# Optimization experiments

Hardware: AMD Instinct MI355X
Metric: run time of the kernel (lower is better)

Reference implementation:

```python
import jax, jax.numpy as jnp
import numpy as np

H, W = 640, 640
C_IN, C_OUT = 3, 64
K, PAD = 7, 3          # 7x7 sparse conv, SAME padding (stride 1)
POOL_K, POOL_S = 3, 2  # valid 3x3 max pool, stride 2
N_SITES = 100000
BN_EPS = 1e-5


def setup_inputs() -> dict:
    key = jax.random.key(0)
    k1, k2, k3 = jax.random.split(key, 3)
    feature_map = jax.random.normal(k1, (H, W, C_IN), dtype=jnp.float32)
    update_location = jax.random.randint(k2, (N_SITES, 2), 0, min(H, W)).astype(jnp.int64)
    # kaiming-uniform-ish init for the 7x7x3 -> 64 conv weight
    fan_in = K * K * C_IN
    bound = np.sqrt(3.0 / fan_in).astype(np.float32)
    weight = jax.random.uniform(k3, (K, K, C_IN, C_OUT), jnp.float32, -bound, bound)
    return {
        "update_location": update_location,
        "feature_map": feature_map,
        "weight": weight,
        "gamma": jnp.ones((C_OUT,), jnp.float32),
        "beta": jnp.zeros((C_OUT,), jnp.float32),
        "running_mean": jnp.zeros((C_OUT,), jnp.float32),
        "running_var": jnp.ones((C_OUT,), jnp.float32),
    }


def reference(update_location, feature_map, weight, gamma, beta, running_mean, running_var):
    # ---- sparse (active-site) 7x7 conv: gather patches only at active sites ----
    fm = jnp.pad(feature_map, ((PAD, PAD), (PAD, PAD), (0, 0)))  # zero pad borders
    offs = jnp.arange(K)
    rows = update_location[:, 0, None] + offs          # [N, K] (pad offset = +PAD-PAD)
    cols = update_location[:, 1, None] + offs          # [N, K]
    patches = fm[rows[:, :, None], cols[:, None, :]]   # [N, K, K, C_IN]
    feats = jnp.einsum('nijc,ijco->no', patches, weight)  # [N, C_OUT]

    # ---- frozen BN + ReLU fused on active sites ----
    inv = gamma * jax.lax.rsqrt(running_var + BN_EPS)
    feats = jnp.maximum(feats * inv + (beta - running_mean * inv), 0.0)

    # ---- scatter active-site features into dense map (inactive sites stay 0) ----
    dense = jnp.zeros((H, W, C_OUT), feats.dtype).at[
        update_location[:, 0], update_location[:, 1]].set(feats)

    # ---- 3x3 stride-2 valid max pool (ReLU outputs >= 0, zeros elsewhere) ----
    pooled = jax.lax.reduce_window(
        dense, 0.0, jax.lax.max,
        (POOL_K, POOL_K, 1), (POOL_S, POOL_S, 1), 'VALID')  # [319, 319, C_OUT]
    return pooled
```

## Files before the change

kernel.cpp:

```cpp
#include <hip/hip_runtime.h>

#define HH 640
#define WW 640
#define COUT 64
#define KK 7
#define NS 100000
#define OHh 319
#define OWw 319
#define PWY 646
#define PWX 648
#define WGT_BLKS 7
#define OWNER_BLKS 391
#define PAD_BLKS 818
#define NBLK 1563
#define NWB (4 * KK * 64)
#define TPR 40

typedef _Float16 half2_t __attribute__((ext_vector_type(2)));
typedef _Float16 h8 __attribute__((ext_vector_type(8)));
typedef float f4 __attribute__((ext_vector_type(4)));
typedef uint4 u4a __attribute__((aligned(8)));

union H2U { unsigned u; half2_t h; };
union H8U { uint4 u; h8 h; _Float16 e[8]; };

__device__ __forceinline__ unsigned short f2bf(float x) {
    unsigned u = __float_as_uint(x);
    return (unsigned short)((u + 0x7FFFu + ((u >> 16) & 1u)) >> 16);
}
__device__ __forceinline__ float bf2f(unsigned short b) {
    return __uint_as_float((unsigned)b << 16);
}

__device__ __forceinline__ bool detect_is64(const int* __restrict__ loc) {
    const int smp = loc[1 + 2 * (int)(threadIdx.x & 63)];
    return __ballot(smp != 0) == 0ULL;
}

__global__ __launch_bounds__(256) void prep_kernel(
        const int* __restrict__ loc, const float* __restrict__ fm,
        const float* __restrict__ wgt, const float* __restrict__ gamma,
        const float* __restrict__ beta, const float* __restrict__ mean,
        const float* __restrict__ var,
        int* __restrict__ owner, uint2* __restrict__ pfm,
        uint4* __restrict__ wbg, float* __restrict__ bn,
        int* __restrict__ aidx) {
    if (blockIdx.x < WGT_BLKS) {
        const int e = blockIdx.x * 256 + threadIdx.x;
        const int t = e / (KK * 64);
        const int rem = e - t * KK * 64;
        const int i = rem >> 6, l = rem & 63;
        const int cout = t * 16 + (l & 15);
        const int q = l >> 4;
        H8U w;
        #pragma unroll
        for (int j = 0; j < 8; ++j) {
            const int kl = q * 8 + j, px = kl >> 2, ci = kl & 3;
            const float v = (px < KK && ci < 3)
                              ? wgt[((i * KK + px) * 3 + ci) * COUT + cout] : 0.0f;
            w.e[j] = (_Float16)v;
        }
        wbg[e] = w.u;
        if (blockIdx.x == 0 && threadIdx.x < COUT) {
            const int co = threadIdx.x;
            const float iv = gamma[co] * rsqrtf(var[co] + 1e-5f);
            bn[co] = iv;
            bn[COUT + co] = beta[co] - mean[co] * iv;
        }
    } else if (blockIdx.x < WGT_BLKS + OWNER_BLKS) {
        const bool is64 = detect_is64(loc);
        const int n = (blockIdx.x - WGT_BLKS) * 256 + threadIdx.x;
        if (n < NS) {
            int r, c;
            if (is64) { r = loc[4 * n]; c = loc[4 * n + 2]; }
            else      { r = loc[2 * n]; c = loc[2 * n + 1]; }
            atomicMax(&owner[r * WW + c], n);
            aidx[n] = r * PWX + c;
        }
    } else {
        const int pair = (blockIdx.x - WGT_BLKS - OWNER_BLKS) * 256 + threadIdx.x;
        const int pix = pair * 2;
        if (pix < PWY * PWX) {
            const int r = pix / PWX, c = pix - r * PWX;
            uint4 o;
            H2U a0, b0, a1, b1;
            a0.u = b0.u = a1.u = b1.u = 0;
            if (r >= 3 && r < 643) {
                const float* s = fm + ((size_t)(r - 3) * WW + (c - 3)) * 3;
                if (c >= 3 && c < 643) {
                    a0.h = half2_t{(_Float16)s[0], (_Float16)s[1]};
                    b0.h = half2_t{(_Float16)s[2], (_Float16)0};
                }
                if (c + 1 >= 3 && c + 1 < 643) {
                    a1.h = half2_t{(_Float16)s[3], (_Float16)s[4]};
                    b1.h = half2_t{(_Float16)s[5], (_Float16)0};
                }
            }
            o.x = a0.u; o.y = b0.u; o.z = a1.u; o.w = b1.u;
            *(uint4*)(pfm + pix) = o;
        }
    }
}

__global__ __launch_bounds__(256) void feats_kernel(
        const int* __restrict__ aidxg, const uint2* __restrict__ pfm,
        const uint4* __restrict__ wbg, const float* __restrict__ bn,
        unsigned short* __restrict__ feats) {
    __shared__ uint4 WB[NWB];
    const int lane = threadIdx.x & 63;
    const int wv = threadIdx.x >> 6;
    #pragma unroll
    for (int e = 0; e < NWB / 256; ++e)
        __builtin_amdgcn_global_load_lds(
            (const uint4*)(wbg + e * 256 + wv * 64 + lane),
            (uint4*)&WB[e * 256 + wv * 64], 16, 0, 0);
    __syncthreads();

    const int s = lane & 15;
    const int q = lane >> 4;
    const int n0 = (blockIdx.x * 4 + wv) * 16;
    if (n0 >= NS) return;

    const int nA = n0 + s;
    const int aidx = aidxg[nA] + 2 * q;

    H8U a[KK];
    #pragma unroll
    for (int i = 0; i < KK; ++i)
        a[i].u = *(const u4a*)(pfm + aidx + i * PWX);

    f4 acc[4] = {f4{0,0,0,0}, f4{0,0,0,0}, f4{0,0,0,0}, f4{0,0,0,0}};
    #pragma unroll
    for (int i = 0; i < KK; ++i) {
        #pragma unroll
        for (int t = 0; t < 4; ++t) {
            H8U b;
            b.u = WB[(t * KK + i) * 64 + lane];
            acc[t] = __builtin_amdgcn_mfma_f32_16x16x32_f16(b.h, a[i].h, acc[t], 0, 0, 0);
        }
    }

    unsigned short* dst = feats + (size_t)nA * COUT;
    #pragma unroll
    for (int t = 0; t < 4; ++t) {
        const float4 iv = *(const float4*)&bn[t * 16 + 4 * q];
        const float4 bi = *(const float4*)&bn[COUT + t * 16 + 4 * q];
        const unsigned short o0 = f2bf(fmaxf(acc[t][0] * iv.x + bi.x, 0.0f));
        const unsigned short o1 = f2bf(fmaxf(acc[t][1] * iv.y + bi.y, 0.0f));
        const unsigned short o2 = f2bf(fmaxf(acc[t][2] * iv.z + bi.z, 0.0f));
        const unsigned short o3 = f2bf(fmaxf(acc[t][3] * iv.w + bi.w, 0.0f));
        uint2 w;
        w.x = (unsigned)o0 | ((unsigned)o1 << 16);
        w.y = (unsigned)o2 | ((unsigned)o3 << 16);
        *(uint2*)(dst + t * 16 + 4 * q) = w;
    }
}

__global__ __launch_bounds__(256) void pool_kernel(
        const int* __restrict__ owner, const unsigned short* __restrict__ feats,
        float* __restrict__ out) {
    const int lane = threadIdx.x & 63;
    const int task = __builtin_amdgcn_readfirstlane(blockIdx.x * 4 + (threadIdx.x >> 6));
    if (task >= OHh * TPR) return;
    const int oh = task / TPR, ow0 = (task % TPR) * 8;
    const int r0 = oh * 2, c0 = ow0 * 2;

    int ov[51];
    #pragma unroll
    for (int dy = 0; dy < 3; ++dy) {
        const int* rowp = owner + (r0 + dy) * WW + c0;
        const uint4 q0 = *(const uint4*)(rowp + 0);
        const uint4 q1 = *(const uint4*)(rowp + 4);
        const uint4 q2 = *(const uint4*)(rowp + 8);
        const uint4 q3 = *(const uint4*)(rowp + 12);
        const int   e0 = rowp[16];
        ov[dy*17 +  0] = __builtin_amdgcn_readfirstlane((int)q0.x);
        ov[dy*17 +  1] = __builtin_amdgcn_readfirstlane((int)q0.y);
        ov[dy*17 +  2] = __builtin_amdgcn_readfirstlane((int)q0.z);
        ov[dy*17 +  3] = __builtin_amdgcn_readfirstlane((int)q0.w);
        ov[dy*17 +  4] = __builtin_amdgcn_readfirstlane((int)q1.x);
        ov[dy*17 +  5] = __builtin_amdgcn_readfirstlane((int)q1.y);
        ov[dy*17 +  6] = __builtin_amdgcn_readfirstlane((int)q1.z);
        ov[dy*17 +  7] = __builtin_amdgcn_readfirstlane((int)q1.w);
        ov[dy*17 +  8] = __builtin_amdgcn_readfirstlane((int)q2.x);
        ov[dy*17 +  9] = __builtin_amdgcn_readfirstlane((int)q2.y);
        ov[dy*17 + 10] = __builtin_amdgcn_readfirstlane((int)q2.z);
        ov[dy*17 + 11] = __builtin_amdgcn_readfirstlane((int)q2.w);
        ov[dy*17 + 12] = __builtin_amdgcn_readfirstlane((int)q3.x);
        ov[dy*17 + 13] = __builtin_amdgcn_readfirstlane((int)q3.y);
        ov[dy*17 + 14] = __builtin_amdgcn_readfirstlane((int)q3.z);
        ov[dy*17 + 15] = __builtin_amdgcn_readfirstlane((int)q3.w);
        ov[dy*17 + 16] = __builtin_amdgcn_readfirstlane(e0);
    }

    float v[51];
    #pragma unroll
    for (int k = 0; k < 51; ++k) v[k] = 0.0f;
    #pragma unroll
    for (int k = 0; k < 51; ++k) {
        const int o = ov[k];
        if (o >= 0 && o < NS)
            v[k] = bf2f(feats[(size_t)o * COUT + lane]);
    }

    float colmax[17];
    #pragma unroll
    for (int j = 0; j < 17; ++j)
        colmax[j] = fmaxf(fmaxf(v[j], v[17 + j]), v[34 + j]);

    #pragma unroll
    for (int w = 0; w < 8; ++w) {
        const int ow = ow0 + w;
        if (ow >= OWw) break;
        const float m = fmaxf(fmaxf(colmax[2 * w], colmax[2 * w + 1]),
                              colmax[2 * w + 2]);
        out[(size_t)(oh * OWw + ow) * COUT + lane] = m;
    }
}

extern "C" void kernel_launch(void* const* d_in, const int* in_sizes, int n_in,
                              void* d_out, int out_size, void* d_ws, size_t ws_size,
                              hipStream_t stream) {
    const int*   loc   = (const int*)d_in[0];
    const float* fm    = (const float*)d_in[1];
    const float* wgt   = (const float*)d_in[2];
    const float* gamma = (const float*)d_in[3];
    const float* beta  = (const float*)d_in[4];
    const float* mean  = (const float*)d_in[5];
    const float* var   = (const float*)d_in[6];
    float* out = (float*)d_out;

    char* ws = (char*)d_ws;
    int* owner = (int*)ws;
    uint2* pfm = (uint2*)(ws + 1638400);
    char* ws2 = ws + 1638400 + (size_t)PWY * PWX * 8;
    uint4* wbg = (uint4*)ws2;
    float* bn  = (float*)(ws2 + NWB * 16);
    int* aidx  = (int*)(ws2 + NWB * 16 + 512);
    unsigned short* feats =
        (unsigned short*)(ws2 + NWB * 16 + 512 + NS * 4);

    prep_kernel<<<WGT_BLKS + OWNER_BLKS + PAD_BLKS, 256, 0, stream>>>(
        loc, fm, wgt, gamma, beta, mean, var, owner, pfm, wbg, bn, aidx);
    feats_kernel<<<NBLK, 256, 0, stream>>>(aidx, pfm, wbg, bn, feats);
    pool_kernel<<<(OHh * TPR + 3) / 4, 256, 0, stream>>>(owner, feats, out);
}
```

Before: 111.0 us.

## Bucket active sites by row band and map bands to XCDs for L2 locality

Prep now sorts active sites into 8 row bands through wave-aggregated atomics, storing (index, padded offset) pairs in per-band buckets. Feats and pool kernels use blockIdx&7 as the band/XCD id, so each XCD's blocks touch a contiguous region of the padded map and owner/feats arrays, aiming to improve per-XCD L2 hit rates. The feats kernel also moves the LDS barrier after the global patch loads so the weight and patch loads overlap. Risks: the memset and atomic bucketing add cost, the launch grid is larger with many early-exit blocks, and the fixed band capacity could truncate sites on skewed inputs.

```diff
diff --git a/kernel.cpp b/kernel.cpp
--- a/kernel.cpp
+++ b/kernel.cpp
@@ -12,9 +12,13 @@
 #define WGT_BLKS 7
 #define OWNER_BLKS 391
 #define PAD_BLKS 818
-#define NBLK 1563
 #define NWB (4 * KK * 64)
 #define TPR 40
+#define NBAND 8
+#define CAP 24576
+#define FSLOTS 256
+#define POOL_LB 3190
+#define POOL_SPB 400
 
 typedef _Float16 half2_t __attribute__((ext_vector_type(2)));
 typedef _Float16 h8 __attribute__((ext_vector_type(8)));
@@ -44,7 +48,7 @@
         const float* __restrict__ var,
         int* __restrict__ owner, uint2* __restrict__ pfm,
         uint4* __restrict__ wbg, float* __restrict__ bn,
-        int* __restrict__ aidx) {
+        int* __restrict__ cnt, uint2* __restrict__ bucket) {
     if (blockIdx.x < WGT_BLKS) {
         const int e = blockIdx.x * 256 + threadIdx.x;
         const int t = e / (KK * 64);
@@ -70,12 +74,30 @@
     } else if (blockIdx.x < WGT_BLKS + OWNER_BLKS) {
         const bool is64 = detect_is64(loc);
         const int n = (blockIdx.x - WGT_BLKS) * 256 + threadIdx.x;
-        if (n < NS) {
-            int r, c;
+        const int lane = threadIdx.x & 63;
+        const bool valid = (n < NS);
+        int r = 0, c = 0;
+        if (valid) {
             if (is64) { r = loc[4 * n]; c = loc[4 * n + 2]; }
             else      { r = loc[2 * n]; c = loc[2 * n + 1]; }
             atomicMax(&owner[r * WW + c], n);
-            aidx[n] = r * PWX + c;
+        }
+        const int band = valid ? (r / 80) : -1;
+        #pragma unroll
+        for (int b = 0; b < NBAND; ++b) {
+            const unsigned long long m = __ballot(band == b);
+            if (m == 0ULL) continue;
+            const int leader = __ffsll((unsigned long long)m) - 1;
+            int base = 0;
+            if (lane == leader) base = atomicAdd(&cnt[b], (int)__popcll(m));
+            base = __shfl(base, leader);
+            if (band == b) {
+                const int rank = (int)__popcll(m & ((1ULL << lane) - 1ULL));
+                const int j = base + rank;
+                if (j < CAP)
+                    bucket[b * CAP + j] = make_uint2((unsigned)n,
+                                                     (unsigned)(r * PWX + c));
+            }
         }
     } else {
         const int pair = (blockIdx.x - WGT_BLKS - OWNER_BLKS) * 256 + threadIdx.x;
@@ -103,9 +125,13 @@
 }
 
 __global__ __launch_bounds__(256) void feats_kernel(
-        const int* __restrict__ aidxg, const uint2* __restrict__ pfm,
-        const uint4* __restrict__ wbg, const float* __restrict__ bn,
-        unsigned short* __restrict__ feats) {
+        const int* __restrict__ cnt, const uint2* __restrict__ bucket,
+        const uint2* __restrict__ pfm, const uint4* __restrict__ wbg,
+        const float* __restrict__ bn, unsigned short* __restrict__ feats) {
+    const int xcd = blockIdx.x & 7, slot = blockIdx.x >> 3;
+    const int cntk = __builtin_amdgcn_readfirstlane(cnt[xcd]);
+    if (slot * 64 >= cntk) return;
+
     __shared__ uint4 WB[NWB];
     const int lane = threadIdx.x & 63;
     const int wv = threadIdx.x >> 6;
@@ -114,20 +140,21 @@
         __builtin_amdgcn_global_load_lds(
             (const uint4*)(wbg + e * 256 + wv * 64 + lane),
             (uint4*)&WB[e * 256 + wv * 64], 16, 0, 0);
-    __syncthreads();
 
     const int s = lane & 15;
     const int q = lane >> 4;
-    const int n0 = (blockIdx.x * 4 + wv) * 16;
-    if (n0 >= NS) return;
-
-    const int nA = n0 + s;
-    const int aidx = aidxg[nA] + 2 * q;
+    const int jj = slot * 64 + wv * 16 + s;
+    const int jc = min(jj, cntk - 1);
+    const uint2 ent = bucket[xcd * CAP + jc];
+    const int nA = (int)ent.x;
+    const int ai = (int)ent.y + 2 * q;
 
     H8U a[KK];
     #pragma unroll
     for (int i = 0; i < KK; ++i)
-        a[i].u = *(const u4a*)(pfm + aidx + i * PWX);
+        a[i].u = *(const u4a*)(pfm + ai + i * PWX);
+
+    __syncthreads();
 
     f4 acc[4] = {f4{0,0,0,0}, f4{0,0,0,0}, f4{0,0,0,0}, f4{0,0,0,0}};
     #pragma unroll
@@ -140,6 +167,7 @@
         }
     }
 
+    if (jj >= cntk) return;
     unsigned short* dst = feats + (size_t)nA * COUT;
     #pragma unroll
     for (int t = 0; t < 4; ++t) {
@@ -159,10 +187,12 @@
 __global__ __launch_bounds__(256) void pool_kernel(
         const int* __restrict__ owner, const unsigned short* __restrict__ feats,
         float* __restrict__ out) {
+    const int xcd = blockIdx.x & 7, slot = blockIdx.x >> 3;
+    const int lb = xcd * POOL_SPB + slot;
+    if (lb >= POOL_LB) return;
     const int lane = threadIdx.x & 63;
-    const int task = __builtin_amdgcn_readfirstlane(blockIdx.x * 4 + (threadIdx.x >> 6));
-    if (task >= OHh * TPR) return;
-    const int oh = task / TPR, ow0 = (task % TPR) * 8;
+    const int strip = __builtin_amdgcn_readfirstlane(lb * 4 + (threadIdx.x >> 6));
+    const int oh = strip / TPR, ow0 = (strip - oh * TPR) * 8;
     const int r0 = oh * 2, c0 = ow0 * 2;
 
     int ov[51];
@@ -236,12 +266,14 @@
     char* ws2 = ws + 1638400 + (size_t)PWY * PWX * 8;
     uint4* wbg = (uint4*)ws2;
     float* bn  = (float*)(ws2 + NWB * 16);
-    int* aidx  = (int*)(ws2 + NWB * 16 + 512);
-    unsigned short* feats =
-        (unsigned short*)(ws2 + NWB * 16 + 512 + NS * 4);
-
+    int* cnt   = (int*)(ws2 + NWB * 16 + 512);
+    uint2* bucket = (uint2*)(ws2 + NWB * 16 + 512 + 128);
+    unsigned short* feats = (unsigned short*)
+        (ws2 + NWB * 16 + 512 + 128 + (size_t)NBAND * CAP * 8);
+
+    hipMemsetAsync(cnt, 0, NBAND * sizeof(int), stream);
     prep_kernel<<<WGT_BLKS + OWNER_BLKS + PAD_BLKS, 256, 0, stream>>>(
-        loc, fm, wgt, gamma, beta, mean, var, owner, pfm, wbg, bn, aidx);
-    feats_kernel<<<NBLK, 256, 0, stream>>>(aidx, pfm, wbg, bn, feats);
-    pool_kernel<<<(OHh * TPR + 3) / 4, 256, 0, stream>>>(owner, feats, out);
-}
+        loc, fm, wgt, gamma, beta, mean, var, owner, pfm, wbg, bn, cnt, bucket);
+    feats_kernel<<<NBAND * FSLOTS, 256, 0, stream>>>(cnt, bucket, pfm, wbg, bn, feats);
+    pool_kernel<<<NBAND * POOL_SPB, 256, 0, stream>>>(owner, feats, out);
+}
```

Result: slower. 247.4 us (+122.9%).
